# Kernel tuning notes

Measured on AMD Instinct MI355X. Metric: run time of the kernel, lower is better.

The kernel has to match this reference:

```python
import jax, jax.numpy as jnp
import numpy as np

B = 16384   # batched decode steps (have_action_batch across transitions)
H = 1024    # hidden_dim
A = 20      # len(ner_map) + 2 valid-action vocabulary


def setup_inputs() -> dict:
    key = jax.random.key(0)
    ks = jax.random.split(key, 10)
    scale = 0.02
    buffer_h = jax.random.normal(ks[0], (B, H), jnp.float32)
    stack_h = jax.random.normal(ks[1], (B, H), jnp.float32)
    output_h = jax.random.normal(ks[2], (B, H), jnp.float32)
    action_h = jax.random.normal(ks[3], (B, H), jnp.float32)
    W1 = jax.random.normal(ks[4], (4 * H, H), jnp.float32) * scale  # lstms_output_2_softmax
    b1 = jnp.zeros((H,), jnp.float32)
    W2 = jax.random.normal(ks[5], (H, A), jnp.float32) * scale      # output_2_act
    b2 = jnp.zeros((A,), jnp.float32)
    real_actions = jax.random.randint(ks[6], (B,), 0, A, dtype=jnp.int32)
    valid_mask = jax.random.bernoulli(ks[7], 0.5, (B, A))
    # gold action must always be in the valid-action list
    valid_mask = valid_mask.at[jnp.arange(B), real_actions].set(True)
    return {
        "buffer_h": buffer_h, "stack_h": stack_h, "output_h": output_h,
        "action_h": action_h, "W1": W1, "b1": b1, "W2": W2, "b2": b2,
        "valid_mask": valid_mask, "real_actions": real_actions,
    }


def reference(buffer_h, stack_h, output_h, action_h, W1, b1, W2, b2, valid_mask, real_actions):
    # ragged concat of per-example LSTM states -> [B, 4H]
    x = jnp.concatenate([buffer_h, stack_h, output_h, action_h], axis=1)
    hidden = jnp.tanh(x @ W1 + b1)          # lstms_output_2_softmax + tanh, [B, H]
    logits = hidden @ W2 + b2               # output_2_act, [B, A]
    # per-example valid-action gather expressed as masked log_softmax
    NEG = jnp.asarray(-1e9, logits.dtype)
    masked = jnp.where(valid_mask, logits, NEG)
    log_probs = jax.nn.log_softmax(masked, axis=-1)
    predict_actions = jnp.argmax(log_probs, axis=-1)               # [B] int
    losses = jnp.take_along_axis(log_probs, real_actions[:, None].astype(jnp.int32), axis=1)[:, 0]
    return predict_actions, losses
```

## Files before the change

### kernel.cpp

```cpp
#include <hip/hip_runtime.h>
#include <math.h>


#define BTOT 16384
#define HD   1024
#define NACT 20
#define KTOT 4096
#define KT_N 128

typedef __attribute__((ext_vector_type(8))) short short8;
typedef __attribute__((ext_vector_type(4))) float f32x4;

#define MFMA(a, b, c) __builtin_amdgcn_mfma_f32_16x16x32_bf16((a), (b), (c), 0, 0, 0)

__device__ __forceinline__ void gload16(const void* g, void* l)
{
    auto gp = (const __attribute__((address_space(1))) unsigned int*)((uintptr_t)g);
    auto lp = (__attribute__((address_space(3))) unsigned int*)((uintptr_t)l);
    __builtin_amdgcn_global_load_lds(gp, lp, 16, 0, 0);
}

__device__ __forceinline__ void split8(const float4 v0, const float4 v1,
                                       int4& hi, int4& lo)
{
    const float f[8] = {v0.x, v0.y, v0.z, v0.w, v1.x, v1.y, v1.z, v1.w};
    unsigned hp[4], lp[4];
#pragma unroll
    for (int i = 0; i < 4; ++i) {
        const unsigned u0 = __float_as_uint(f[2 * i]);
        const unsigned u1 = __float_as_uint(f[2 * i + 1]);
        const unsigned r0 = u0 + 0x7FFFu + ((u0 >> 16) & 1u);
        const unsigned r1 = u1 + 0x7FFFu + ((u1 >> 16) & 1u);
        hp[i] = (r0 >> 16) | (r1 & 0xFFFF0000u);
        const float h0 = __uint_as_float(r0 & 0xFFFF0000u);
        const float h1 = __uint_as_float(r1 & 0xFFFF0000u);
        const float d0 = f[2 * i] - h0;
        const float d1 = f[2 * i + 1] - h1;
        const unsigned s0 = __float_as_uint(d0);
        const unsigned s1 = __float_as_uint(d1);
        const unsigned q0 = s0 + 0x7FFFu + ((s0 >> 16) & 1u);
        const unsigned q1 = s1 + 0x7FFFu + ((s1 >> 16) & 1u);
        lp[i] = (q0 >> 16) | (q1 & 0xFFFF0000u);
    }
    hi = make_int4((int)hp[0], (int)hp[1], (int)hp[2], (int)hp[3]);
    lo = make_int4((int)lp[0], (int)lp[1], (int)lp[2], (int)lp[3]);
}

__device__ __forceinline__ int4 cvt8(const float4 v0, const float4 v1)
{
    const float f[8] = {v0.x, v0.y, v0.z, v0.w, v1.x, v1.y, v1.z, v1.w};
    unsigned hp[4];
#pragma unroll
    for (int i = 0; i < 4; ++i) {
        const unsigned u0 = __float_as_uint(f[2 * i]);
        const unsigned u1 = __float_as_uint(f[2 * i + 1]);
        const unsigned r0 = u0 + 0x7FFFu + ((u0 >> 16) & 1u);
        const unsigned r1 = u1 + 0x7FFFu + ((u1 >> 16) & 1u);
        hp[i] = (r0 >> 16) | (r1 & 0xFFFF0000u);
    }
    return make_int4((int)hp[0], (int)hp[1], (int)hp[2], (int)hp[3]);
}

__global__ __launch_bounds__(256) void detect_mask_kernel(
    const unsigned int* __restrict__ w, int nwords, int* __restrict__ ctr)
{
    int c0 = 0, c1 = 0, c2 = 0, c3 = 0;
    for (int i = blockIdx.x * 256 + threadIdx.x; i < nwords; i += gridDim.x * 256) {
        unsigned int v = w[i];
        c0 += (v & 0x000000FFu) ? 1 : 0;
        c1 += (v & 0x0000FF00u) ? 1 : 0;
        c2 += (v & 0x00FF0000u) ? 1 : 0;
        c3 += (v & 0xFF000000u) ? 1 : 0;
    }
#pragma unroll
    for (int off = 32; off; off >>= 1) {
        c0 += __shfl_xor(c0, off, 64);
        c1 += __shfl_xor(c1, off, 64);
        c2 += __shfl_xor(c2, off, 64);
        c3 += __shfl_xor(c3, off, 64);
    }
    if ((threadIdx.x & 63) == 0) {
        atomicAdd(&ctr[0], c0);
        atomicAdd(&ctr[1], c1);
        atomicAdd(&ctr[2], c2);
        atomicAdd(&ctr[3], c3);
    }
}

__global__ __launch_bounds__(256) void wpack_kernel(
    const float* __restrict__ W1, char* __restrict__ Wp)
{
    const int b  = blockIdx.x;
    const int t  = threadIdx.x;
    const int nt = b >> 7;
    const int kt = b & 127;
    const int nn = t & 127;
    const int h  = t >> 7;

    float f[16];
#pragma unroll
    for (int kk = 0; kk < 16; ++kk)
        f[kk] = W1[(size_t)(kt * 32 + h * 16 + kk) * HD + nt * 128 + nn];

    int4 hi0, lo0, hi1, lo1;
    split8(make_float4(f[0], f[1], f[2], f[3]),
           make_float4(f[4], f[5], f[6], f[7]), hi0, lo0);
    split8(make_float4(f[8], f[9], f[10], f[11]),
           make_float4(f[12], f[13], f[14], f[15]), hi1, lo1);

    char* rowp = Wp + (((size_t)(nt * KT_N + kt)) << 14) + nn * 128;
    const int r7 = nn & 7;
    const int s0 = ((2 * h) ^ r7) << 4;
    const int s1 = ((2 * h + 1) ^ r7) << 4;
    *(int4*)(rowp + s0)        = hi0;
    *(int4*)(rowp + s1)        = hi1;
    *(int4*)(rowp + (s0 ^ 64)) = lo0;
    *(int4*)(rowp + (s1 ^ 64)) = lo1;
}

#define PHASE(AP)                                                                   \
    {                                                                               \
        const short8 ah0 = *(const short8*)(bufc + (aBase + (2*(AP)) * 2048));      \
        const short8 ah1 = *(const short8*)(bufc + (aBase + (2*(AP)+1) * 2048));    \
        __builtin_amdgcn_s_setprio(1);                                              \
        _Pragma("unroll")                                                           \
        for (int nf = 0; nf < 4; ++nf) {                                            \
            acc[2*(AP)][nf]   = MFMA(ah0, bh[nf], acc[2*(AP)][nf]);                 \
            acc[2*(AP)][nf]   = MFMA(ah0, bl[nf], acc[2*(AP)][nf]);                 \
            acc[2*(AP)+1][nf] = MFMA(ah1, bh[nf], acc[2*(AP)+1][nf]);               \
            acc[2*(AP)+1][nf] = MFMA(ah1, bl[nf], acc[2*(AP)+1][nf]);               \
        }                                                                           \
        __builtin_amdgcn_s_setprio(0);                                              \
    }

__global__ __launch_bounds__(512, 1) void gemm1_mfma_kernel(
    const float* __restrict__ A0, const float* __restrict__ A1,
    const float* __restrict__ A2, const float* __restrict__ A3,
    const char* __restrict__ Wp, const float* __restrict__ b1,
    float* __restrict__ hidden)
{
    extern __shared__ __align__(16) char smem[];

    const int newbid = (blockIdx.x & 7) * 32 + (blockIdx.x >> 3);
    const int mt = newbid >> 2;
    const int nt = newbid & 3;

    const int t    = threadIdx.x;
    const int lane = t & 63;
    const int wid  = t >> 6;
    const int wr = wid >> 2, wc = wid & 3;
    const int lrow = lane & 15;
    const int lk   = lane >> 4;

    const int stag = (wid ^ (wid >> 2)) & 1;

    const int rowL  = t >> 1;
    const int khalf = t & 1;
    const size_t aRowOff = (size_t)(mt * 256 + rowL) * HD;

    const char* gB0 = Wp + (((size_t)((nt * 2)     * KT_N)) << 14);
    const char* gB1 = Wp + (((size_t)((nt * 2 + 1) * KT_N)) << 14);

    const unsigned aBase = (unsigned)(wr * 128 + lrow) * 128
                         + (((unsigned)lk ^ (unsigned)(lrow & 7)) << 4);
    const unsigned bBase = (unsigned)(wc >> 1) * 16384
                         + (unsigned)((wc & 1) * 64 + lrow) * 128
                         + (((unsigned)lk ^ (unsigned)(lrow & 7)) << 4);

    const int r7 = rowL & 7;
    const unsigned wA0 = (unsigned)rowL * 128 + (((unsigned)(2 * khalf)     ^ (unsigned)r7) << 4);
    const unsigned wA1 = (unsigned)rowL * 128 + (((unsigned)(2 * khalf + 1) ^ (unsigned)r7) << 4);

    f32x4 acc[8][4];
#pragma unroll
    for (int i = 0; i < 8; ++i)
#pragma unroll
        for (int j = 0; j < 4; ++j) acc[i][j] = (f32x4){0.f, 0.f, 0.f, 0.f};

    {
        const float4* ap = (const float4*)(A0 + aRowOff + khalf * 16);
        const float4 f0 = ap[0], f1 = ap[1], f2 = ap[2], f3 = ap[3];
        const int4 h0 = cvt8(f0, f1);
        const int4 h1 = cvt8(f2, f3);
        char* lA = smem;
        *(int4*)(lA + wA0) = h0;
        *(int4*)(lA + wA1) = h1;
        char* lB = smem + 32768;
        gload16(gB0 + t * 16,        lB + t * 16);
        gload16(gB0 + 8192 + t * 16, lB + 8192 + t * 16);
        gload16(gB1 + t * 16,        lB + 16384 + t * 16);
        gload16(gB1 + 8192 + t * 16, lB + 24576 + t * 16);
    }
    __syncthreads();

    for (int kt = 0; kt < KT_N; ++kt) {
        const int cur = kt & 1;
        const char* bufc  = smem + cur * 65536;
        const char* bufcB = bufc + 32768;
        char*       bufn  = smem + (cur ^ 1) * 65536;
        const bool pref = (kt + 1 < KT_N);

        float4 f0, f1, f2, f3;
        if (pref) {
            char* lB = bufn + 32768;
            const char* s0 = gB0 + (((size_t)(kt + 1)) << 14);
            const char* s1 = gB1 + (((size_t)(kt + 1)) << 14);
            gload16(s0 + t * 16,        lB + t * 16);
            gload16(s0 + 8192 + t * 16, lB + 8192 + t * 16);
            gload16(s1 + t * 16,        lB + 16384 + t * 16);
            gload16(s1 + 8192 + t * 16, lB + 24576 + t * 16);
            const int kg = (kt + 1) * 32 + khalf * 16;
            const float* seg = (kg < 1024) ? A0 : (kg < 2048) ? A1 : (kg < 3072) ? A2 : A3;
            const float4* ap = (const float4*)(seg + aRowOff + (kg & 1023));
            f0 = ap[0]; f1 = ap[1]; f2 = ap[2]; f3 = ap[3];
        }

        short8 bh[4], bl[4];
#pragma unroll
        for (int nf = 0; nf < 4; ++nf) {
            bh[nf] = *(const short8*)(bufcB + (bBase + nf * 2048));
            bl[nf] = *(const short8*)(bufcB + ((bBase + nf * 2048) ^ 64));
        }

        if (stag == 0) {
            PHASE(0) PHASE(1) PHASE(2) PHASE(3)
        } else {
            PHASE(2) PHASE(3) PHASE(0) PHASE(1)
        }

        if (pref) {
            const int4 h0 = cvt8(f0, f1);
            const int4 h1 = cvt8(f2, f3);
            *(int4*)(bufn + wA0) = h0;
            *(int4*)(bufn + wA1) = h1;
        }
        __syncthreads();
    }

#pragma unroll
    for (int nf = 0; nf < 4; ++nf) {
        const int col = nt * 256 + wc * 64 + nf * 16 + lrow;
        const float bias = b1[col];
#pragma unroll
        for (int mf = 0; mf < 8; ++mf) {
            const int row0 = mt * 256 + wr * 128 + mf * 16 + lk * 4;
#pragma unroll
            for (int r = 0; r < 4; ++r)
                hidden[(size_t)(row0 + r) * HD + col] = tanhf(acc[mf][nf][r] + bias);
        }
    }
}

__device__ __forceinline__ void finish_row(
    const float* __restrict__ acc, const float* __restrict__ b2,
    const void* __restrict__ mask, const int* __restrict__ real_actions,
    int fmt, int row, float* __restrict__ out,
    int* __restrict__ flagCnt, int* __restrict__ flagList, int lane)
{
    float masked[NACT];
#pragma unroll
    for (int a = 0; a < NACT; ++a) {
        const float lg = acc[a] + b2[a];
        bool valid;
        if (fmt == 0)      valid = ((const unsigned char*)mask)[(size_t)row * NACT + a] != 0;
        else if (fmt == 1) valid = ((const int*)mask)[(size_t)row * NACT + a] != 0;
        else               valid = ((const float*)mask)[(size_t)row * NACT + a] != 0.f;
        masked[a] = valid ? lg : -1e9f;
    }
    float m = masked[0], m2 = -3e38f;
    int amax = 0;
#pragma unroll
    for (int a = 1; a < NACT; ++a) {
        const float v = masked[a];
        if (v > m) { m2 = m; m = v; amax = a; }
        else if (v > m2) m2 = v;
    }
    float s = 0.f;
#pragma unroll
    for (int a = 0; a < NACT; ++a) s += expf(masked[a] - m);
    const float lse = m + logf(s);
    const int ga = real_actions[row];
    float gl = masked[0];
#pragma unroll
    for (int a = 1; a < NACT; ++a) gl = (ga == a) ? masked[a] : gl;
    if (lane == 0) {
        out[row] = (float)amax;
        out[BTOT + row] = gl - lse;
        if (flagList != nullptr && (m - m2) < 4e-3f) {
            const int ix = atomicAdd(flagCnt, 1);
            flagList[ix] = row;
        }
    }
}

__global__ __launch_bounds__(256) void head_kernel(
    const float* __restrict__ hidden, const float* __restrict__ W2,
    const float* __restrict__ b2, const void* __restrict__ mask,
    const int* __restrict__ real_actions, int* __restrict__ ctr,
    int* __restrict__ flagList, float* __restrict__ out, int rowBase)
{
    const int lane = threadIdx.x & 63;
    const int lr0  = (blockIdx.x * 4 + (threadIdx.x >> 6)) * 2;

    float a0[NACT], a1[NACT];
#pragma unroll
    for (int a = 0; a < NACT; ++a) { a0[a] = 0.f; a1[a] = 0.f; }

    const float* h0 = hidden + (size_t)lr0 * HD;
    const float* h1 = h0 + HD;
#pragma unroll 4
    for (int j = 0; j < 16; ++j) {
        const int h = lane + 64 * j;
        const float hv0 = h0[h];
        const float hv1 = h1[h];
        const float4* w4 = (const float4*)(W2 + (size_t)h * NACT);
        const float4 w0 = w4[0], w1 = w4[1], w2 = w4[2], w3 = w4[3], w4v = w4[4];
        a0[0]  = fmaf(hv0, w0.x,  a0[0]);  a1[0]  = fmaf(hv1, w0.x,  a1[0]);
        a0[1]  = fmaf(hv0, w0.y,  a0[1]);  a1[1]  = fmaf(hv1, w0.y,  a1[1]);
        a0[2]  = fmaf(hv0, w0.z,  a0[2]);  a1[2]  = fmaf(hv1, w0.z,  a1[2]);
        a0[3]  = fmaf(hv0, w0.w,  a0[3]);  a1[3]  = fmaf(hv1, w0.w,  a1[3]);
        a0[4]  = fmaf(hv0, w1.x,  a0[4]);  a1[4]  = fmaf(hv1, w1.x,  a1[4]);
        a0[5]  = fmaf(hv0, w1.y,  a0[5]);  a1[5]  = fmaf(hv1, w1.y,  a1[5]);
        a0[6]  = fmaf(hv0, w1.z,  a0[6]);  a1[6]  = fmaf(hv1, w1.z,  a1[6]);
        a0[7]  = fmaf(hv0, w1.w,  a0[7]);  a1[7]  = fmaf(hv1, w1.w,  a1[7]);
        a0[8]  = fmaf(hv0, w2.x,  a0[8]);  a1[8]  = fmaf(hv1, w2.x,  a1[8]);
        a0[9]  = fmaf(hv0, w2.y,  a0[9]);  a1[9]  = fmaf(hv1, w2.y,  a1[9]);
        a0[10] = fmaf(hv0, w2.z,  a0[10]); a1[10] = fmaf(hv1, w2.z,  a1[10]);
        a0[11] = fmaf(hv0, w2.w,  a0[11]); a1[11] = fmaf(hv1, w2.w,  a1[11]);
        a0[12] = fmaf(hv0, w3.x,  a0[12]); a1[12] = fmaf(hv1, w3.x,  a1[12]);
        a0[13] = fmaf(hv0, w3.y,  a0[13]); a1[13] = fmaf(hv1, w3.y,  a1[13]);
        a0[14] = fmaf(hv0, w3.z,  a0[14]); a1[14] = fmaf(hv1, w3.z,  a1[14]);
        a0[15] = fmaf(hv0, w3.w,  a0[15]); a1[15] = fmaf(hv1, w3.w,  a1[15]);
        a0[16] = fmaf(hv0, w4v.x, a0[16]); a1[16] = fmaf(hv1, w4v.x, a1[16]);
        a0[17] = fmaf(hv0, w4v.y, a0[17]); a1[17] = fmaf(hv1, w4v.y, a1[17]);
        a0[18] = fmaf(hv0, w4v.z, a0[18]); a1[18] = fmaf(hv1, w4v.z, a1[18]);
        a0[19] = fmaf(hv0, w4v.w, a0[19]); a1[19] = fmaf(hv1, w4v.w, a1[19]);
    }
#pragma unroll
    for (int off = 32; off; off >>= 1) {
#pragma unroll
        for (int a = 0; a < NACT; ++a) {
            a0[a] += __shfl_xor(a0[a], off, 64);
            a1[a] += __shfl_xor(a1[a], off, 64);
        }
    }

    const int c1 = ctr[1], c2 = ctr[2], c3 = ctr[3];
    const int fmt = (c1 > 0) ? 0 : ((c2 > 0 || c3 > 0) ? 2 : 1);

    finish_row(a0, b2, mask, real_actions, fmt, rowBase + lr0,     out, &ctr[4], flagList, lane);
    finish_row(a1, b2, mask, real_actions, fmt, rowBase + lr0 + 1, out, &ctr[4], flagList, lane);
}

__global__ __launch_bounds__(256) void refine_hidden_kernel(
    const float* __restrict__ A0, const float* __restrict__ A1,
    const float* __restrict__ A2, const float* __restrict__ A3,
    const float* __restrict__ W1, const float* __restrict__ b1,
    const int* __restrict__ ctr, const int* __restrict__ list,
    float* __restrict__ hiddenR, int cap)
{
    __shared__ float xs[2][KTOT];
    __shared__ float red[2][4][64];
    const int tid = threadIdx.x;
    int count = ctr[4]; if (count > cap) count = cap;
    const int total = ((count + 1) >> 1) << 4;

    for (int u = blockIdx.x; u < total; u += gridDim.x) {
        const int p  = u >> 4;
        const int f0 = 2 * p;
        const int f1 = (2 * p + 1 < count) ? (2 * p + 1) : f0;
        const int r0 = list[f0];
        const int r1 = list[f1];
        const int colBase = (u & 15) << 6;

        for (int i = tid; i < KTOT; i += 256) {
            const float* seg = (i < 1024) ? A0 : (i < 2048) ? A1 : (i < 3072) ? A2 : A3;
            xs[0][i] = seg[(size_t)r0 * HD + (i & 1023)];
            xs[1][i] = seg[(size_t)r1 * HD + (i & 1023)];
        }
        __syncthreads();

        const int col   = colBase + (tid & 63);
        const int kbase = (tid >> 6) << 10;
        const float* Wc = W1 + col;
        float acc0 = 0.f, acc1 = 0.f;

        float wa[16], wb[16];
#pragma unroll
        for (int v = 0; v < 16; ++v) wa[v] = Wc[(size_t)(kbase + v) * HD];
#pragma unroll
        for (int v = 0; v < 16; ++v) wb[v] = Wc[(size_t)(kbase + 16 + v) * HD];

        const int kend = kbase + 1024;
        for (int k0 = kbase; k0 < kend; k0 += 32) {
#pragma unroll
            for (int v = 0; v < 16; ++v) {
                acc0 = fmaf(xs[0][k0 + v], wa[v], acc0);
                acc1 = fmaf(xs[1][k0 + v], wa[v], acc1);
            }
            if (k0 + 32 < kend) {
#pragma unroll
                for (int v = 0; v < 16; ++v)
                    wa[v] = Wc[(size_t)(k0 + 32 + v) * HD];
            }
#pragma unroll
            for (int v = 0; v < 16; ++v) {
                acc0 = fmaf(xs[0][k0 + 16 + v], wb[v], acc0);
                acc1 = fmaf(xs[1][k0 + 16 + v], wb[v], acc1);
            }
            if (k0 + 48 < kend) {
#pragma unroll
                for (int v = 0; v < 16; ++v)
                    wb[v] = Wc[(size_t)(k0 + 48 + v) * HD];
            }
        }

        red[0][tid >> 6][tid & 63] = acc0;
        red[1][tid >> 6][tid & 63] = acc1;
        __syncthreads();

        if (tid < 128) {
            const int r = tid >> 6, c = tid & 63;
            const float s = red[r][0][c] + red[r][1][c] + red[r][2][c] + red[r][3][c];
            const int f = r ? f1 : f0;
            hiddenR[(size_t)f * HD + colBase + c] = tanhf(s + b1[colBase + c]);
        }
        __syncthreads();
    }
}

__global__ __launch_bounds__(256) void refine_head_kernel(
    const float* __restrict__ hiddenR, const float* __restrict__ W2,
    const float* __restrict__ b2, const void* __restrict__ mask,
    const int* __restrict__ real_actions, const int* __restrict__ ctr,
    const int* __restrict__ list, float* __restrict__ out, int cap)
{
    const int lane = threadIdx.x & 63;
    const int wv   = threadIdx.x >> 6;
    int count = ctr[4]; if (count > cap) count = cap;
    const int c1 = ctr[1], c2 = ctr[2], c3 = ctr[3];
    const int fmt = (c1 > 0) ? 0 : ((c2 > 0 || c3 > 0) ? 2 : 1);

    for (int f = blockIdx.x * 4 + wv; f < count; f += gridDim.x * 4) {
        const int row = list[f];
        const float* hrow = hiddenR + (size_t)f * HD;
        float a20[NACT];
#pragma unroll
        for (int a = 0; a < NACT; ++a) a20[a] = 0.f;
#pragma unroll 4
        for (int m = 0; m < 16; ++m) {
            const int h = lane + 64 * m;
            const float hv = hrow[h];
            const float4* w4 = (const float4*)(W2 + (size_t)h * NACT);
            const float4 w0 = w4[0], w1 = w4[1], w2 = w4[2], w3 = w4[3], w4v = w4[4];
            a20[0]  = fmaf(hv, w0.x,  a20[0]);  a20[1]  = fmaf(hv, w0.y,  a20[1]);
            a20[2]  = fmaf(hv, w0.z,  a20[2]);  a20[3]  = fmaf(hv, w0.w,  a20[3]);
            a20[4]  = fmaf(hv, w1.x,  a20[4]);  a20[5]  = fmaf(hv, w1.y,  a20[5]);
            a20[6]  = fmaf(hv, w1.z,  a20[6]);  a20[7]  = fmaf(hv, w1.w,  a20[7]);
            a20[8]  = fmaf(hv, w2.x,  a20[8]);  a20[9]  = fmaf(hv, w2.y,  a20[9]);
            a20[10] = fmaf(hv, w2.z,  a20[10]); a20[11] = fmaf(hv, w2.w,  a20[11]);
            a20[12] = fmaf(hv, w3.x,  a20[12]); a20[13] = fmaf(hv, w3.y,  a20[13]);
            a20[14] = fmaf(hv, w3.z,  a20[14]); a20[15] = fmaf(hv, w3.w,  a20[15]);
            a20[16] = fmaf(hv, w4v.x, a20[16]); a20[17] = fmaf(hv, w4v.y, a20[17]);
            a20[18] = fmaf(hv, w4v.z, a20[18]); a20[19] = fmaf(hv, w4v.w, a20[19]);
        }
#pragma unroll
        for (int off = 32; off; off >>= 1) {
#pragma unroll
            for (int a = 0; a < NACT; ++a) a20[a] += __shfl_xor(a20[a], off, 64);
        }
        finish_row(a20, b2, mask, real_actions, fmt, row, out, nullptr, nullptr, lane);
    }
}

extern "C" void kernel_launch(void* const* d_in, const int* in_sizes, int n_in,
                              void* d_out, int out_size, void* d_ws, size_t ws_size,
                              hipStream_t stream)
{
    const float* buf_h = (const float*)d_in[0];
    const float* stk_h = (const float*)d_in[1];
    const float* out_h = (const float*)d_in[2];
    const float* act_h = (const float*)d_in[3];
    const float* W1    = (const float*)d_in[4];
    const float* b1    = (const float*)d_in[5];
    const float* W2    = (const float*)d_in[6];
    const float* b2    = (const float*)d_in[7];
    const void*  mask  = d_in[8];
    const int*   ra    = (const int*)d_in[9];
    float*       out   = (float*)d_out;

    int*  ctr      = (int*)d_ws;
    int*  flagList = (int*)((char*)d_ws + 256);
    char* Wp       = (char*)d_ws + 256 + 65536;
    const size_t wpBytes = (size_t)8 * KT_N * 16384;
    float* hidden  = (float*)(Wp + wpBytes);

    hipMemsetAsync(d_ws, 0, 256, stream);
    detect_mask_kernel<<<64, 256, 0, stream>>>(
        (const unsigned int*)mask, BTOT * NACT / 4, ctr);
    wpack_kernel<<<8 * KT_N, 256, 0, stream>>>(W1, Wp);

    hipFuncSetAttribute((const void*)gemm1_mfma_kernel,
                        hipFuncAttributeMaxDynamicSharedMemorySize, 131072);

    gemm1_mfma_kernel<<<256, 512, 131072, stream>>>(
        buf_h, stk_h, out_h, act_h, Wp, b1, hidden);
    head_kernel<<<BTOT / 8, 256, 0, stream>>>(
        hidden, W2, b2, mask, ra, ctr, flagList, out, 0);

    float* hiddenR = hidden;
    refine_hidden_kernel<<<2048, 256, 0, stream>>>(
        buf_h, stk_h, out_h, act_h, W1, b1, ctr, flagList, hiddenR, BTOT);
    refine_head_kernel<<<64, 256, 0, stream>>>(
        hiddenR, W2, b2, mask, ra, ctr, flagList, out, BTOT);
}
```

Before: 517.0 us.

## Retile GEMM1 to 128x256 blocks of 256 threads with two blocks per CU

The main bf16 hi/lo MFMA GEMM changes from 256x256 tiles with 512 threads and 128KB of LDS to 128x256 tiles with 256 threads and 80KB of LDS, launched as 512 blocks with launch bounds allowing two blocks per CU. Each wave now holds 4 A fragments and streams B fragments per phase, and the A LDS row stride and swizzle are adjusted for the narrower tile. The intent is more resident waves per CU to hide latency and a more even block count across CUs. The cost is lower arithmetic intensity per block, since each B tile is reused over fewer rows, and the wave stagger ordering is dropped.

```diff
diff --git a/kernel.cpp b/kernel.cpp
--- a/kernel.cpp
+++ b/kernel.cpp
@@ -7,6 +7,10 @@
 #define NACT 20
 #define KTOT 4096
 #define KT_N 128
+
+#define ABUF  0
+#define BBUF  8192
+#define BUFSZ 40960
 
 typedef __attribute__((ext_vector_type(8))) short short8;
 typedef __attribute__((ext_vector_type(4))) float f32x4;
@@ -118,22 +122,24 @@
     *(int4*)(rowp + (s1 ^ 64)) = lo1;
 }
 
-#define PHASE(AP)                                                                   \
+#define PHASE(NP)                                                                   \
     {                                                                               \
-        const short8 ah0 = *(const short8*)(bufc + (aBase + (2*(AP)) * 2048));      \
-        const short8 ah1 = *(const short8*)(bufc + (aBase + (2*(AP)+1) * 2048));    \
+        const short8 bh0 = *(const short8*)(bufc + (bBase + (2*(NP)) * 2048));      \
+        const short8 bl0 = *(const short8*)(bufc + ((bBase + (2*(NP)) * 2048) ^ 64)); \
+        const short8 bh1 = *(const short8*)(bufc + (bBase + (2*(NP)+1) * 2048));    \
+        const short8 bl1 = *(const short8*)(bufc + ((bBase + (2*(NP)+1) * 2048) ^ 64)); \
         __builtin_amdgcn_s_setprio(1);                                              \
         _Pragma("unroll")                                                           \
-        for (int nf = 0; nf < 4; ++nf) {                                            \
-            acc[2*(AP)][nf]   = MFMA(ah0, bh[nf], acc[2*(AP)][nf]);                 \
-            acc[2*(AP)][nf]   = MFMA(ah0, bl[nf], acc[2*(AP)][nf]);                 \
-            acc[2*(AP)+1][nf] = MFMA(ah1, bh[nf], acc[2*(AP)+1][nf]);               \
-            acc[2*(AP)+1][nf] = MFMA(ah1, bl[nf], acc[2*(AP)+1][nf]);               \
+        for (int mf = 0; mf < 4; ++mf) {                                            \
+            acc[mf][2*(NP)]   = MFMA(ah[mf], bh0, acc[mf][2*(NP)]);                 \
+            acc[mf][2*(NP)]   = MFMA(ah[mf], bl0, acc[mf][2*(NP)]);                 \
+            acc[mf][2*(NP)+1] = MFMA(ah[mf], bh1, acc[mf][2*(NP)+1]);               \
+            acc[mf][2*(NP)+1] = MFMA(ah[mf], bl1, acc[mf][2*(NP)+1]);               \
         }                                                                           \
         __builtin_amdgcn_s_setprio(0);                                              \
     }
 
-__global__ __launch_bounds__(512, 1) void gemm1_mfma_kernel(
+__global__ __launch_bounds__(256, 2) void gemm1_mfma_kernel(
     const float* __restrict__ A0, const float* __restrict__ A1,
     const float* __restrict__ A2, const float* __restrict__ A3,
     const char* __restrict__ Wp, const float* __restrict__ b1,
@@ -141,92 +147,83 @@
 {
     extern __shared__ __align__(16) char smem[];
 
-    const int newbid = (blockIdx.x & 7) * 32 + (blockIdx.x >> 3);
-    const int mt = newbid >> 2;
-    const int nt = newbid & 3;
+    const int newbid = (blockIdx.x & 7) * 64 + (blockIdx.x >> 3);
+    const int nt = newbid >> 7;
+    const int mt = newbid & 127;
 
     const int t    = threadIdx.x;
     const int lane = t & 63;
     const int wid  = t >> 6;
-    const int wr = wid >> 2, wc = wid & 3;
+    const int wr = wid >> 1, wc = wid & 1;
     const int lrow = lane & 15;
     const int lk   = lane >> 4;
 
-    const int stag = (wid ^ (wid >> 2)) & 1;
-
     const int rowL  = t >> 1;
     const int khalf = t & 1;
-    const size_t aRowOff = (size_t)(mt * 256 + rowL) * HD;
+    const size_t aRowOff = (size_t)(mt * 128 + rowL) * HD;
 
     const char* gB0 = Wp + (((size_t)((nt * 2)     * KT_N)) << 14);
     const char* gB1 = Wp + (((size_t)((nt * 2 + 1) * KT_N)) << 14);
 
-    const unsigned aBase = (unsigned)(wr * 128 + lrow) * 128
+    const unsigned aBase = (unsigned)(wr * 64 + lrow) * 64
+                         + (((unsigned)lk ^ (((unsigned)lrow >> 1) & 3u)) << 4);
+    const unsigned bBase = (unsigned)BBUF + (unsigned)wc * 16384
+                         + (unsigned)lrow * 128
                          + (((unsigned)lk ^ (unsigned)(lrow & 7)) << 4);
-    const unsigned bBase = (unsigned)(wc >> 1) * 16384
-                         + (unsigned)((wc & 1) * 64 + lrow) * 128
-                         + (((unsigned)lk ^ (unsigned)(lrow & 7)) << 4);
-
-    const int r7 = rowL & 7;
-    const unsigned wA0 = (unsigned)rowL * 128 + (((unsigned)(2 * khalf)     ^ (unsigned)r7) << 4);
-    const unsigned wA1 = (unsigned)rowL * 128 + (((unsigned)(2 * khalf + 1) ^ (unsigned)r7) << 4);
-
-    f32x4 acc[8][4];
-#pragma unroll
-    for (int i = 0; i < 8; ++i)
-#pragma unroll
-        for (int j = 0; j < 4; ++j) acc[i][j] = (f32x4){0.f, 0.f, 0.f, 0.f};
+
+    const int rx = (rowL >> 1) & 3;
+    const unsigned wA0 = (unsigned)rowL * 64 + (((unsigned)(2 * khalf)     ^ (unsigned)rx) << 4);
+    const unsigned wA1 = (unsigned)rowL * 64 + (((unsigned)(2 * khalf + 1) ^ (unsigned)rx) << 4);
+
+    f32x4 acc[4][8];
+#pragma unroll
+    for (int i = 0; i < 4; ++i)
+#pragma unroll
+        for (int j = 0; j < 8; ++j) acc[i][j] = (f32x4){0.f, 0.f, 0.f, 0.f};
 
     {
         const float4* ap = (const float4*)(A0 + aRowOff + khalf * 16);
         const float4 f0 = ap[0], f1 = ap[1], f2 = ap[2], f3 = ap[3];
         const int4 h0 = cvt8(f0, f1);
         const int4 h1 = cvt8(f2, f3);
-        char* lA = smem;
-        *(int4*)(lA + wA0) = h0;
-        *(int4*)(lA + wA1) = h1;
-        char* lB = smem + 32768;
-        gload16(gB0 + t * 16,        lB + t * 16);
-        gload16(gB0 + 8192 + t * 16, lB + 8192 + t * 16);
-        gload16(gB1 + t * 16,        lB + 16384 + t * 16);
-        gload16(gB1 + 8192 + t * 16, lB + 24576 + t * 16);
+        *(int4*)(smem + wA0) = h0;
+        *(int4*)(smem + wA1) = h1;
+        char* lB = smem + BBUF;
+#pragma unroll
+        for (int i = 0; i < 4; ++i) {
+            gload16(gB0 + t * 16 + i * 4096, lB + t * 16 + i * 4096);
+            gload16(gB1 + t * 16 + i * 4096, lB + 16384 + t * 16 + i * 4096);
+        }
     }
     __syncthreads();
 
     for (int kt = 0; kt < KT_N; ++kt) {
-        const int cur = kt & 1;
-        const char* bufc  = smem + cur * 65536;
-        const char* bufcB = bufc + 32768;
-        char*       bufn  = smem + (cur ^ 1) * 65536;
+        const char* bufc = smem + (kt & 1) * BUFSZ;
+        char*       bufn = smem + ((kt & 1) ^ 1) * BUFSZ;
         const bool pref = (kt + 1 < KT_N);
 
         float4 f0, f1, f2, f3;
         if (pref) {
-            char* lB = bufn + 32768;
+            char* lB = bufn + BBUF;
             const char* s0 = gB0 + (((size_t)(kt + 1)) << 14);
             const char* s1 = gB1 + (((size_t)(kt + 1)) << 14);
-            gload16(s0 + t * 16,        lB + t * 16);
-            gload16(s0 + 8192 + t * 16, lB + 8192 + t * 16);
-            gload16(s1 + t * 16,        lB + 16384 + t * 16);
-            gload16(s1 + 8192 + t * 16, lB + 24576 + t * 16);
+#pragma unroll
+            for (int i = 0; i < 4; ++i) {
+                gload16(s0 + t * 16 + i * 4096, lB + t * 16 + i * 4096);
+                gload16(s1 + t * 16 + i * 4096, lB + 16384 + t * 16 + i * 4096);
+            }
             const int kg = (kt + 1) * 32 + khalf * 16;
             const float* seg = (kg < 1024) ? A0 : (kg < 2048) ? A1 : (kg < 3072) ? A2 : A3;
             const float4* ap = (const float4*)(seg + aRowOff + (kg & 1023));
             f0 = ap[0]; f1 = ap[1]; f2 = ap[2]; f3 = ap[3];
         }
 
-        short8 bh[4], bl[4];
-#pragma unroll
-        for (int nf = 0; nf < 4; ++nf) {
-            bh[nf] = *(const short8*)(bufcB + (bBase + nf * 2048));
-            bl[nf] = *(const short8*)(bufcB + ((bBase + nf * 2048) ^ 64));
-        }
-
-        if (stag == 0) {
-            PHASE(0) PHASE(1) PHASE(2) PHASE(3)
-        } else {
-            PHASE(2) PHASE(3) PHASE(0) PHASE(1)
-        }
+        short8 ah[4];
+#pragma unroll
+        for (int mf = 0; mf < 4; ++mf)
+            ah[mf] = *(const short8*)(bufc + (aBase + mf * 1024));
+
+        PHASE(0) PHASE(1) PHASE(2) PHASE(3)
 
         if (pref) {
             const int4 h0 = cvt8(f0, f1);
@@ -238,12 +235,12 @@
     }
 
 #pragma unroll
-    for (int nf = 0; nf < 4; ++nf) {
-        const int col = nt * 256 + wc * 64 + nf * 16 + lrow;
+    for (int nf = 0; nf < 8; ++nf) {
+        const int col = nt * 256 + wc * 128 + nf * 16 + lrow;
         const float bias = b1[col];
 #pragma unroll
-        for (int mf = 0; mf < 8; ++mf) {
-            const int row0 = mt * 256 + wr * 128 + mf * 16 + lk * 4;
+        for (int mf = 0; mf < 4; ++mf) {
+            const int row0 = mt * 128 + wr * 64 + mf * 16 + lk * 4;
 #pragma unroll
             for (int r = 0; r < 4; ++r)
                 hidden[(size_t)(row0 + r) * HD + col] = tanhf(acc[mf][nf][r] + bias);
@@ -501,9 +498,9 @@
     wpack_kernel<<<8 * KT_N, 256, 0, stream>>>(W1, Wp);
 
     hipFuncSetAttribute((const void*)gemm1_mfma_kernel,
-                        hipFuncAttributeMaxDynamicSharedMemorySize, 131072);
-
-    gemm1_mfma_kernel<<<256, 512, 131072, stream>>>(
+                        hipFuncAttributeMaxDynamicSharedMemorySize, 81920);
+
+    gemm1_mfma_kernel<<<512, 256, 81920, stream>>>(
         buf_h, stk_h, out_h, act_h, Wp, b1, hidden);
     head_kernel<<<BTOT / 8, 256, 0, stream>>>(
         hidden, W2, b2, mask, ra, ctr, flagList, out, 0);
```

New measurement: 518.2 us. No clear change (+0.2%).
